# Optimization experiments

Hardware: AMD Instinct MI355X
Metric: run time of the kernel (lower is better)

## Reference

```python
import jax, jax.numpy as jnp
import numpy as np

IN_FEATURES = 4096
OUT_FEATURES = 4096
ACTIVE_IN = 1024
ACTIVE_OUT = 1024
BATCH, SEQ = 4, 2048


def setup_inputs() -> dict:
    key = jax.random.key(0)
    kx, kw, kb = jax.random.split(key, 3)
    x = jax.random.normal(kx, (BATCH, SEQ, IN_FEATURES), dtype=jnp.float32)
    # nn.Linear default init scale ~ 1/sqrt(fan_in)
    W = jax.random.normal(kw, (ACTIVE_OUT, ACTIVE_IN), dtype=jnp.float32) / np.sqrt(ACTIVE_IN)
    b = jax.random.normal(kb, (ACTIVE_OUT,), dtype=jnp.float32) / np.sqrt(ACTIVE_IN)
    rng = np.random.default_rng(42)
    # unique sorted index subsets (faithful to pruning-style selection; scatter is write-once)
    in_idx = jnp.asarray(np.sort(rng.choice(IN_FEATURES, ACTIVE_IN, replace=False)), dtype=jnp.int32)
    out_idx = jnp.asarray(np.sort(rng.choice(OUT_FEATURES, ACTIVE_OUT, replace=False)), dtype=jnp.int32)
    return {"x": x, "W": W, "b": b, "in_idx": in_idx, "out_idx": out_idx}


def reference(x, W, b, in_idx, out_idx):
    # gather active input columns: [B, S, ACTIVE_IN]
    x_active = jnp.take(x, in_idx, axis=-1)
    # dense linear: y = x_active @ W.T + b -> [B, S, ACTIVE_OUT]
    y = jnp.einsum('bsi,oi->bso', x_active, W) + b
    # scatter into zero-initialized full output buffer: [B, S, OUT_FEATURES]
    out = jnp.zeros(x.shape[:-1] + (OUT_FEATURES,), dtype=y.dtype)
    out = out.at[..., out_idx].set(y)
    return out
```

## Files before the change

kernel.cpp:

```cpp
#include <hip/hip_runtime.h>
#include <hip/hip_bf16.h>


typedef unsigned short u16;
typedef u16   u16x4 __attribute__((ext_vector_type(4)));
typedef int   i32x4 __attribute__((ext_vector_type(4)));
typedef float f32x4 __attribute__((ext_vector_type(4)));
typedef __bf16 bf16x8 __attribute__((ext_vector_type(8)));

constexpr int IN_F  = 4096;
constexpr int OUT_F = 4096;
constexpr int AI    = 1024;
constexpr int AO    = 1024;
constexpr int M_ROWS = 4 * 2048;
constexpr int BK    = 32;
constexpr int NKT   = AI / BK;

__device__ __forceinline__ u16 f2bf(float f) {
    union { __hip_bfloat16 h; u16 u; } cv;
    cv.h = __float2bfloat16(f);
    return cv.u;
}
__device__ __forceinline__ float bf2f(u16 u) {
    union { float f; unsigned int i; } cv;
    cv.i = ((unsigned int)u) << 16;
    return cv.f;
}

__global__ __launch_bounds__(256)
void gather_kernel(const float* __restrict__ x,
                   const int* __restrict__ in_idx,
                   const float* __restrict__ W,
                   const int* __restrict__ out_idx,
                   u16* __restrict__ Wb, int* __restrict__ pos,
                   u16* __restrict__ Xa) {
    __shared__ float xrow[IN_F];
    const int m = blockIdx.x;
    const int t = threadIdx.x;
    if (m < 1024) {
        const int t2 = m * 256 + t;
        if (t2 < AO) pos[out_idx[t2]] = t2;
        f32x4 w = reinterpret_cast<const f32x4*>(W)[t2];
        u16x4 wv;
        wv.x = f2bf(w.x); wv.y = f2bf(w.y); wv.z = f2bf(w.z); wv.w = f2bf(w.w);
        reinterpret_cast<u16x4*>(Wb)[t2] = wv;
    }
    const f32x4* src = reinterpret_cast<const f32x4*>(x + (size_t)m * IN_F);
#pragma unroll
    for (int i = 0; i < 4; ++i)
        *reinterpret_cast<f32x4*>(&xrow[i * 1024 + t * 4]) = src[i * 256 + t];
    __syncthreads();
    i32x4 idx = reinterpret_cast<const i32x4*>(in_idx)[t];
    u16x4 v;
    v.x = f2bf(xrow[idx.x]);
    v.y = f2bf(xrow[idx.y]);
    v.z = f2bf(xrow[idx.z]);
    v.w = f2bf(xrow[idx.w]);
    reinterpret_cast<u16x4*>(Xa + (size_t)m * AI)[t] = v;
}

__global__ __launch_bounds__(256, 4)
void gemmfw_kernel(const u16* __restrict__ Xa, const u16* __restrict__ Wb,
                   const float* __restrict__ bias,
                   const int* __restrict__ out_idx,
                   const int* __restrict__ pos, float* __restrict__ out) {
    __shared__ char L[128 * 136 * 2];
    const int t    = threadIdx.x;
    const int wid  = t >> 6;
    const int lane = t & 63;
    const int n_lo = lane & 15;
    const int kg   = lane >> 4;
    const int orig = blockIdx.x;
    const int wgid = (orig & 7) * 64 + (orig >> 3);
    const int mb = wgid >> 3, nb = wgid & 7;
    const int m0 = mb * 128, n0 = nb * 128;
    const int wm = wid >> 1, wn = wid & 1;

    const int r16 = lane >> 2;
    const int c8  = (lane & 3) * 8;
    auto stage = [&](int buf, int k0) {
#pragma unroll
        for (int h = 0; h < 2; ++h) {
            const int row = h * 64 + wid * 16 + r16;
            const int db  = (h * 64 + wid * 16) * 64;
            __builtin_amdgcn_global_load_lds(
                (const __attribute__((address_space(1))) void*)
                    (Xa + (size_t)(m0 + row) * AI + k0 + c8),
                (__attribute__((address_space(3))) void*)(L + buf * 8192 + db),
                16, 0, 0);
            __builtin_amdgcn_global_load_lds(
                (const __attribute__((address_space(1))) void*)
                    (Wb + (size_t)(n0 + row) * AI + k0 + c8),
                (__attribute__((address_space(3))) void*)(L + 16384 + buf * 8192 + db),
                16, 0, 0);
        }
    };

    f32x4 acc[4][4];
#pragma unroll
    for (int i = 0; i < 4; ++i)
#pragma unroll
        for (int j = 0; j < 4; ++j) acc[i][j] = (f32x4)0.0f;

    stage(0, 0);
    int buf = 0;
    for (int kt = 0; kt < NKT; ++kt) {
        __syncthreads();
        if (kt + 1 < NKT) stage(buf ^ 1, (kt + 1) * BK);
        bf16x8 a[4], b[4];
#pragma unroll
        for (int i = 0; i < 4; ++i)
            a[i] = *reinterpret_cast<const bf16x8*>(
                L + buf * 8192 + (wm * 64 + i * 16 + n_lo) * 64 + kg * 16);
#pragma unroll
        for (int j = 0; j < 4; ++j)
            b[j] = *reinterpret_cast<const bf16x8*>(
                L + 16384 + buf * 8192 + (wn * 64 + j * 16 + n_lo) * 64 + kg * 16);
#pragma unroll
        for (int i = 0; i < 4; ++i)
#pragma unroll
            for (int j = 0; j < 4; ++j)
                acc[i][j] = __builtin_amdgcn_mfma_f32_16x16x32_bf16(
                    a[i], b[j], acc[i][j], 0, 0, 0);
        buf ^= 1;
    }

    float bv[4];
#pragma unroll
    for (int j = 0; j < 4; ++j) bv[j] = bias[n0 + wn * 64 + j * 16 + n_lo];

    __syncthreads();
    u16* ys = reinterpret_cast<u16*>(L);
#pragma unroll
    for (int i = 0; i < 4; ++i)
#pragma unroll
        for (int j = 0; j < 4; ++j)
#pragma unroll
            for (int r = 0; r < 4; ++r)
                ys[(wm * 64 + i * 16 + kg * 4 + r) * 136 +
                   wn * 64 + j * 16 + n_lo] = f2bf(acc[i][j][r] + bv[j]);
    __syncthreads();

    const int lo = (nb == 0) ? 0 : out_idx[nb * 128];
    const int hi = (nb == 7) ? OUT_F : out_idx[(nb + 1) * 128];
    const int s4 = (lo + 3) >> 2;
    const int e4 = hi >> 2;
    const i32x4* pos4 = reinterpret_cast<const i32x4*>(pos);
    const int rg = t >> 5, j32 = t & 31;
#pragma unroll 1
    for (int rr = 0; rr < 128; rr += 8) {
        const int row = rr + rg;
        float* orow = out + (size_t)(m0 + row) * OUT_F;
        const u16* yr = ys + row * 136;
        for (int c = lo + j32; c < s4 * 4; c += 32) {
            int p = pos[c];
            orow[c] = (p >= 0) ? bf2f(yr[p - n0]) : 0.0f;
        }
        for (int c4 = s4 + j32; c4 < e4; c4 += 32) {
            i32x4 p = pos4[c4];
            f32x4 v;
            v.x = (p.x >= 0) ? bf2f(yr[p.x - n0]) : 0.0f;
            v.y = (p.y >= 0) ? bf2f(yr[p.y - n0]) : 0.0f;
            v.z = (p.z >= 0) ? bf2f(yr[p.z - n0]) : 0.0f;
            v.w = (p.w >= 0) ? bf2f(yr[p.w - n0]) : 0.0f;
            reinterpret_cast<f32x4*>(orow)[c4] = v;
        }
        for (int c = e4 * 4 + j32; c < hi; c += 32) {
            int p = pos[c];
            orow[c] = (p >= 0) ? bf2f(yr[p - n0]) : 0.0f;
        }
    }
}

extern "C" void kernel_launch(void* const* d_in, const int* in_sizes, int n_in,
                              void* d_out, int out_size, void* d_ws, size_t ws_size,
                              hipStream_t stream) {
    const float* x      = (const float*)d_in[0];
    const float* W      = (const float*)d_in[1];
    const float* b      = (const float*)d_in[2];
    const int*   in_idx = (const int*)d_in[3];
    const int*   out_idx= (const int*)d_in[4];
    float* out = (float*)d_out;

    char* ws = (char*)d_ws;
    int* pos = (int*)ws;
    u16* Wb  = (u16*)(ws + 16384);
    u16* Xa  = (u16*)(ws + 16384 + 2 * 1024 * 1024);

    hipMemsetAsync(pos, 0xFF, OUT_F * sizeof(int), stream);
    gather_kernel<<<M_ROWS, 256, 0, stream>>>(x, in_idx, W, out_idx, Wb, pos, Xa);
    gemmfw_kernel<<<(M_ROWS / 128) * (AO / 128), 256, 0, stream>>>(
        Xa, Wb, b, out_idx, pos, out);
}
```

Measured before the change: 281.5 us.

## Scatter GEMM results directly to output after zero-filling the column range

The epilogue no longer stages bf16 results in LDS and gathers them through a position map. Each block now zero-fills its output column range with vector stores, synchronises, and then scatters fp32 accumulator-plus-bias values straight to out_idx columns. This drops the pos memset, the pos build in the gather kernel, and the bf16 rounding of outputs. The cost is scattered scalar 4-byte global stores and every active column being written twice, which relies on ordering between threads of the same block inside the row range.

```diff
diff --git a/kernel.cpp b/kernel.cpp
--- a/kernel.cpp
+++ b/kernel.cpp
@@ -21,25 +21,18 @@
     cv.h = __float2bfloat16(f);
     return cv.u;
 }
-__device__ __forceinline__ float bf2f(u16 u) {
-    union { float f; unsigned int i; } cv;
-    cv.i = ((unsigned int)u) << 16;
-    return cv.f;
-}
 
 __global__ __launch_bounds__(256)
 void gather_kernel(const float* __restrict__ x,
                    const int* __restrict__ in_idx,
                    const float* __restrict__ W,
-                   const int* __restrict__ out_idx,
-                   u16* __restrict__ Wb, int* __restrict__ pos,
+                   u16* __restrict__ Wb,
                    u16* __restrict__ Xa) {
     __shared__ float xrow[IN_F];
     const int m = blockIdx.x;
     const int t = threadIdx.x;
     if (m < 1024) {
         const int t2 = m * 256 + t;
-        if (t2 < AO) pos[out_idx[t2]] = t2;
         f32x4 w = reinterpret_cast<const f32x4*>(W)[t2];
         u16x4 wv;
         wv.x = f2bf(w.x); wv.y = f2bf(w.y); wv.z = f2bf(w.z); wv.w = f2bf(w.w);
@@ -63,8 +56,8 @@
 void gemmfw_kernel(const u16* __restrict__ Xa, const u16* __restrict__ Wb,
                    const float* __restrict__ bias,
                    const int* __restrict__ out_idx,
-                   const int* __restrict__ pos, float* __restrict__ out) {
-    __shared__ char L[128 * 136 * 2];
+                   float* __restrict__ out) {
+    __shared__ char L[4 * 8192];
     const int t    = threadIdx.x;
     const int wid  = t >> 6;
     const int lane = t & 63;
@@ -125,49 +118,41 @@
         buf ^= 1;
     }
 
-    float bv[4];
-#pragma unroll
-    for (int j = 0; j < 4; ++j) bv[j] = bias[n0 + wn * 64 + j * 16 + n_lo];
-
-    __syncthreads();
-    u16* ys = reinterpret_cast<u16*>(L);
-#pragma unroll
-    for (int i = 0; i < 4; ++i)
-#pragma unroll
-        for (int j = 0; j < 4; ++j)
-#pragma unroll
-            for (int r = 0; r < 4; ++r)
-                ys[(wm * 64 + i * 16 + kg * 4 + r) * 136 +
-                   wn * 64 + j * 16 + n_lo] = f2bf(acc[i][j][r] + bv[j]);
-    __syncthreads();
-
     const int lo = (nb == 0) ? 0 : out_idx[nb * 128];
     const int hi = (nb == 7) ? OUT_F : out_idx[(nb + 1) * 128];
     const int s4 = (lo + 3) >> 2;
     const int e4 = hi >> 2;
-    const i32x4* pos4 = reinterpret_cast<const i32x4*>(pos);
     const int rg = t >> 5, j32 = t & 31;
+    const f32x4 z4 = (f32x4)0.0f;
 #pragma unroll 1
     for (int rr = 0; rr < 128; rr += 8) {
         const int row = rr + rg;
         float* orow = out + (size_t)(m0 + row) * OUT_F;
-        const u16* yr = ys + row * 136;
-        for (int c = lo + j32; c < s4 * 4; c += 32) {
-            int p = pos[c];
-            orow[c] = (p >= 0) ? bf2f(yr[p - n0]) : 0.0f;
-        }
-        for (int c4 = s4 + j32; c4 < e4; c4 += 32) {
-            i32x4 p = pos4[c4];
-            f32x4 v;
-            v.x = (p.x >= 0) ? bf2f(yr[p.x - n0]) : 0.0f;
-            v.y = (p.y >= 0) ? bf2f(yr[p.y - n0]) : 0.0f;
-            v.z = (p.z >= 0) ? bf2f(yr[p.z - n0]) : 0.0f;
-            v.w = (p.w >= 0) ? bf2f(yr[p.w - n0]) : 0.0f;
-            reinterpret_cast<f32x4*>(orow)[c4] = v;
-        }
-        for (int c = e4 * 4 + j32; c < hi; c += 32) {
-            int p = pos[c];
-            orow[c] = (p >= 0) ? bf2f(yr[p - n0]) : 0.0f;
+        for (int c = lo + j32; c < s4 * 4; c += 32) orow[c] = 0.0f;
+        for (int c4 = s4 + j32; c4 < e4; c4 += 32)
+            reinterpret_cast<f32x4*>(orow)[c4] = z4;
+        for (int c = e4 * 4 + j32; c < hi; c += 32) orow[c] = 0.0f;
+    }
+
+    __syncthreads();
+
+    int   oj[4];
+    float bv[4];
+#pragma unroll
+    for (int j = 0; j < 4; ++j) {
+        const int jg = n0 + wn * 64 + j * 16 + n_lo;
+        oj[j] = out_idx[jg];
+        bv[j] = bias[jg];
+    }
+#pragma unroll
+    for (int i = 0; i < 4; ++i) {
+        const int rbase = m0 + wm * 64 + i * 16 + kg * 4;
+#pragma unroll
+        for (int r = 0; r < 4; ++r) {
+            float* orow = out + (size_t)(rbase + r) * OUT_F;
+#pragma unroll
+            for (int j = 0; j < 4; ++j)
+                orow[oj[j]] = acc[i][j][r] + bv[j];
         }
     }
 }
@@ -183,12 +168,10 @@
     float* out = (float*)d_out;
 
     char* ws = (char*)d_ws;
-    int* pos = (int*)ws;
-    u16* Wb  = (u16*)(ws + 16384);
-    u16* Xa  = (u16*)(ws + 16384 + 2 * 1024 * 1024);
+    u16* Wb  = (u16*)ws;
+    u16* Xa  = (u16*)(ws + 2 * 1024 * 1024);
 
-    hipMemsetAsync(pos, 0xFF, OUT_F * sizeof(int), stream);
-    gather_kernel<<<M_ROWS, 256, 0, stream>>>(x, in_idx, W, out_idx, Wb, pos, Xa);
+    gather_kernel<<<M_ROWS, 256, 0, stream>>>(x, in_idx, W, Wb, Xa);
     gemmfw_kernel<<<(M_ROWS / 128) * (AO / 128), 256, 0, stream>>>(
-        Xa, Wb, b, out_idx, pos, out);
+        Xa, Wb, b, out_idx, out);
 }
```

New measurement: 283.4 us. About the same (+0.7%).
